# Kernel tuning notes

Measured on AMD Instinct MI355X. Metric: run time of the kernel, lower is better.

## Reference

```python
import jax, jax.numpy as jnp
import numpy as np

B, H, N, D = 16, 2048, 1024, 2048  # batch, seq len, vocab_size, d_model (= 2*vocab)
KAPPA = 1.0
SCALE = 0.02  # std for materialized params (original inits to zeros -> trivial output)


def setup_inputs() -> dict:
    key = jax.random.key(0)
    kz, kf, kv, kw = jax.random.split(key, 4)
    z = jax.random.randint(kz, (B, H), 0, N)
    F_mat = jax.random.normal(kf, (D, D), jnp.float32) * SCALE
    V = jax.random.normal(kv, (D, D), jnp.float32) * SCALE
    W = jax.random.normal(kw, (D, D), jnp.float32) * SCALE
    return {"z": z, "F_mat": F_mat, "V": V, "W": W}


def reference(z, F_mat, V, W):
    # x[b,t] = e_{z[b,t]} + e_{N + z[b,t-1]},  x[b,0] = e_{z[b,0]}  (E / E_tilde basis rows)
    z_prev = jnp.roll(z, 1, axis=1).at[:, 0].set(0)
    E_z = jax.nn.one_hot(z, D, dtype=jnp.float32)          # [B,H,D]
    x = E_z + jax.nn.one_hot(z_prev + N, D, dtype=jnp.float32)
    x = x.at[:, 0, :].set(E_z[:, 0, :])

    x_H = x[:, -1, :]                                      # [B,D] single query
    W_x = jnp.einsum('bhd,ed->bhe', x, W)                  # x @ W.T -> [B,H,D]
    scores = jnp.einsum('bd,bhd->bh', x_H, W_x)            # [B,H]
    attn = jax.nn.softmax(scores, axis=-1)                 # att_type='softmax'
    weighted_sum = jnp.einsum('bh,bhd->bd', attn, x)       # [B,D]

    # U.T @ (.) just takes the first N coordinates (U = E.T, identity columns)
    xi_A = (weighted_sum @ V.T)[:, :N]                     # [B,N]
    combined = x_H + KAPPA * weighted_sum
    xi_F = (combined @ F_mat.T)[:, :N]                     # [B,N]
    xi = xi_A + xi_F
    # match torch output shape [B, N, 1]
    return xi[..., None], xi_A[..., None], xi_F[..., None]
```

## Files before the change

### kernel.cpp

```cpp
#include <hip/hip_runtime.h>

#define BB 16
#define HH 2048
#define NN 1024
#define DD 2048
#define DG4 (DD / 4)


__device__ __forceinline__ unsigned short f2bf(float f) {
    unsigned u = __float_as_uint(f);
    u += 0x7fffu + ((u >> 16) & 1u);
    return (unsigned short)(u >> 16);
}

__global__ __launch_bounds__(512) void ot_p1warm(const int* __restrict__ z,
                                                 const float* __restrict__ Fm,
                                                 const float* __restrict__ Vm,
                                                 const float* __restrict__ Wm,
                                                 int* __restrict__ hdr,
                                                 uint2* __restrict__ wsB) {
    __shared__ int   zsh[HH];
    __shared__ float u[DD];
    __shared__ float wsf[DD];
    __shared__ float redt[8];

    const int tid  = threadIdx.x;
    const int lane = tid & 63;
    const int w    = tid >> 6;
    const int g    = blockIdx.x;

    float4 pf[8];
    {
        const int r = w >> 1, m = w & 1;
        const float4* __restrict__ src =
            (const float4*)((m ? Fm : Vm) + (size_t)(4 * g + r) * DD);
#pragma unroll
        for (int k = 0; k < 8; ++k) pf[k] = src[k * 64 + lane];
    }

    if (g < BB) {
        const int b = g;
        const int4 zt = ((const int4*)(z + (size_t)b * HH))[DG4 - 1];
        const int d1 = zt.w;
        const int d2 = zt.z + NN;

        const int4 zv = ((const int4*)(z + (size_t)b * HH))[tid];
        float4 wa = ((const float4*)(Wm + (size_t)d1 * DD))[tid];
        float4 wc = ((const float4*)(Wm + (size_t)d2 * DD))[tid];

        ((int4*)zsh)[tid] = zv;
        float4 uu;
        uu.x = wa.x + wc.x; uu.y = wa.y + wc.y;
        uu.z = wa.z + wc.z; uu.w = wa.w + wc.w;
        ((float4*)u)[tid] = uu;
        ((float4*)wsf)[tid] = make_float4(0.f, 0.f, 0.f, 0.f);
        __syncthreads();

        const int zp0 = (tid > 0) ? zsh[4 * tid - 1] + NN : 0;
        const float s0 = u[zv.x] + ((tid > 0) ? u[zp0] : 0.f);
        const float s1 = u[zv.y] + u[zv.x + NN];
        const float s2 = u[zv.z] + u[zv.y + NN];
        const float s3 = u[zv.w] + u[zv.z + NN];

        const float e0 = __expf(s0);
        const float e1 = __expf(s1);
        const float e2 = __expf(s2);
        const float e3 = __expf(s3);
        float t = (e0 + e1) + (e2 + e3);
#pragma unroll
        for (int off = 32; off > 0; off >>= 1) t += __shfl_xor(t, off);
        if (lane == 0) redt[w] = t;

        atomicAdd(&wsf[zv.x], e0);
        if (tid > 0) atomicAdd(&wsf[zp0], e0);
        atomicAdd(&wsf[zv.y], e1); atomicAdd(&wsf[zv.x + NN], e1);
        atomicAdd(&wsf[zv.z], e2); atomicAdd(&wsf[zv.y + NN], e2);
        atomicAdd(&wsf[zv.w], e3); atomicAdd(&wsf[zv.z + NN], e3);
        __syncthreads();

        float tot = redt[0];
#pragma unroll
        for (int i = 1; i < 8; ++i) tot += redt[i];
        const float inv = 1.f / tot;

        uint2 p;
        p.x = (unsigned)f2bf(wsf[4 * tid + 0] * inv)
            | ((unsigned)f2bf(wsf[4 * tid + 1] * inv) << 16);
        p.y = (unsigned)f2bf(wsf[4 * tid + 2] * inv)
            | ((unsigned)f2bf(wsf[4 * tid + 3] * inv) << 16);
        wsB[(size_t)tid * BB + b] = p;
        if (tid == 0) { hdr[b] = d1; hdr[BB + b] = d2; }
    }

#pragma unroll
    for (int k = 0; k < 8; ++k)
        asm volatile("" :: "v"(pf[k].x), "v"(pf[k].y), "v"(pf[k].z), "v"(pf[k].w));
}

__global__ __launch_bounds__(512, 4) void ot_phase2(const float* __restrict__ V,
                                                    const float* __restrict__ F,
                                                    const int* __restrict__ hdr,
                                                    const uint2* __restrict__ wsB,
                                                    float* __restrict__ out) {
    const int tid  = threadIdx.x;
    const int lane = tid & 63;
    const int w    = tid >> 6;
    const int b    = lane & 15;
    const int s    = tid >> 4;
    const int g    = blockIdx.x;

    uint2 wsr[16];
#pragma unroll
    for (int i = 0; i < 16; ++i) wsr[i] = wsB[(size_t)(s + 32 * i) * BB + b];

    const float4* __restrict__ Vr0 = (const float4*)(V + (size_t)(4 * g + 0) * DD);
    const float4* __restrict__ Vr1 = (const float4*)(V + (size_t)(4 * g + 1) * DD);
    const float4* __restrict__ Vr2 = (const float4*)(V + (size_t)(4 * g + 2) * DD);
    const float4* __restrict__ Vr3 = (const float4*)(V + (size_t)(4 * g + 3) * DD);
    const float4* __restrict__ Fr0 = (const float4*)(F + (size_t)(4 * g + 0) * DD);
    const float4* __restrict__ Fr1 = (const float4*)(F + (size_t)(4 * g + 1) * DD);
    const float4* __restrict__ Fr2 = (const float4*)(F + (size_t)(4 * g + 2) * DD);
    const float4* __restrict__ Fr3 = (const float4*)(F + (size_t)(4 * g + 3) * DD);

    float acc[8];
#pragma unroll
    for (int j = 0; j < 8; ++j) acc[j] = 0.f;

#pragma unroll
    for (int it = 0; it < 16; ++it) {
        const int dg = s + 32 * it;
        const uint2 p = wsr[it];
        const float s0 = __uint_as_float(p.x << 16);
        const float s1 = __uint_as_float(p.x & 0xffff0000u);
        const float s2 = __uint_as_float(p.y << 16);
        const float s3 = __uint_as_float(p.y & 0xffff0000u);
        float4 v0 = Vr0[dg], v1 = Vr1[dg], v2 = Vr2[dg], v3 = Vr3[dg];
        float4 f0 = Fr0[dg], f1 = Fr1[dg], f2 = Fr2[dg], f3 = Fr3[dg];
        acc[0] += v0.x * s0 + v0.y * s1 + v0.z * s2 + v0.w * s3;
        acc[1] += f0.x * s0 + f0.y * s1 + f0.z * s2 + f0.w * s3;
        acc[2] += v1.x * s0 + v1.y * s1 + v1.z * s2 + v1.w * s3;
        acc[3] += f1.x * s0 + f1.y * s1 + f1.z * s2 + f1.w * s3;
        acc[4] += v2.x * s0 + v2.y * s1 + v2.z * s2 + v2.w * s3;
        acc[5] += f2.x * s0 + f2.y * s1 + f2.z * s2 + f2.w * s3;
        acc[6] += v3.x * s0 + v3.y * s1 + v3.z * s2 + v3.w * s3;
        acc[7] += f3.x * s0 + f3.y * s1 + f3.z * s2 + f3.w * s3;
    }

#pragma unroll
    for (int j = 0; j < 8; ++j) {
        float p = acc[j];
        p += __shfl_xor(p, 16);
        p += __shfl_xor(p, 32);
        acc[j] = p;
    }

    __shared__ float red[8][8][BB];
    if (lane < 16) {
#pragma unroll
        for (int j = 0; j < 8; ++j) red[j][w][b] = acc[j];
    }
    __syncthreads();

    if (tid < 64) {
        const int r = tid >> 4, bb = tid & 15;
        float A = 0.f, Fv = 0.f;
#pragma unroll
        for (int ww = 0; ww < 8; ++ww) {
            A  += red[2 * r + 0][ww][bb];
            Fv += red[2 * r + 1][ww][bb];
        }
        const int n = 4 * g + r;
        const float* __restrict__ Fr = F + (size_t)n * DD;
        Fv += Fr[hdr[bb]] + Fr[hdr[BB + bb]];
        out[(size_t)bb * NN + n]            = A + Fv;
        out[(size_t)(BB + bb) * NN + n]     = A;
        out[(size_t)(2 * BB + bb) * NN + n] = Fv;
    }
}

extern "C" void kernel_launch(void* const* d_in, const int* in_sizes, int n_in,
                              void* d_out, int out_size, void* d_ws, size_t ws_size,
                              hipStream_t stream) {
    const int*   z  = (const int*)d_in[0];
    const float* Fm = (const float*)d_in[1];
    const float* Vm = (const float*)d_in[2];
    const float* Wm = (const float*)d_in[3];
    float* out = (float*)d_out;

    int*   hdr = (int*)d_ws;
    uint2* wsB = (uint2*)((char*)d_ws + 128);

    ot_p1warm<<<256, 512, 0, stream>>>(z, Fm, Vm, Wm, hdr, wsB);
    ot_phase2<<<NN / 4, 512, 0, stream>>>(Vm, Fm, hdr, wsB, out);
}
```

Before: 23.73 us.

## Fuse softmax and projection kernels into one launch with a global flag barrier

Merges the two kernels into a single 256-block launch. The 16 batch blocks publish their bf16 attention weights with atomic stores and bump a release counter, and every block spins on that flag before running the V/F row projection. This removes the second kernel launch and the gap between kernels. In exchange it adds a memset, a spin-wait whose budget can expire, and a dependence on all 256 blocks being co-resident, which is a deadlock or correctness risk.

```diff
diff --git a/kernel.cpp b/kernel.cpp
--- a/kernel.cpp
+++ b/kernel.cpp
@@ -13,16 +13,19 @@
     return (unsigned short)(u >> 16);
 }
 
-__global__ __launch_bounds__(512) void ot_p1warm(const int* __restrict__ z,
-                                                 const float* __restrict__ Fm,
-                                                 const float* __restrict__ Vm,
-                                                 const float* __restrict__ Wm,
-                                                 int* __restrict__ hdr,
-                                                 uint2* __restrict__ wsB) {
+__global__ __launch_bounds__(512) void ot_one(const int* __restrict__ z,
+                                              const float* __restrict__ Fm,
+                                              const float* __restrict__ Vm,
+                                              const float* __restrict__ Wm,
+                                              unsigned* __restrict__ flag,
+                                              int* __restrict__ hdr,
+                                              unsigned long long* __restrict__ wsB,
+                                              float* __restrict__ out) {
     __shared__ int   zsh[HH];
     __shared__ float u[DD];
     __shared__ float wsf[DD];
     __shared__ float redt[8];
+    __shared__ float red[8][8][BB];
 
     const int tid  = threadIdx.x;
     const int lane = tid & 63;
@@ -39,12 +42,12 @@
     }
 
     if (g < BB) {
-        const int b = g;
-        const int4 zt = ((const int4*)(z + (size_t)b * HH))[DG4 - 1];
+        const int b0 = g;
+        const int4 zt = ((const int4*)(z + (size_t)b0 * HH))[DG4 - 1];
         const int d1 = zt.w;
         const int d2 = zt.z + NN;
 
-        const int4 zv = ((const int4*)(z + (size_t)b * HH))[tid];
+        const int4 zv = ((const int4*)(z + (size_t)b0 * HH))[tid];
         float4 wa = ((const float4*)(Wm + (size_t)d1 * DD))[tid];
         float4 wc = ((const float4*)(Wm + (size_t)d2 * DD))[tid];
 
@@ -83,44 +86,53 @@
         for (int i = 1; i < 8; ++i) tot += redt[i];
         const float inv = 1.f / tot;
 
-        uint2 p;
-        p.x = (unsigned)f2bf(wsf[4 * tid + 0] * inv)
-            | ((unsigned)f2bf(wsf[4 * tid + 1] * inv) << 16);
-        p.y = (unsigned)f2bf(wsf[4 * tid + 2] * inv)
-            | ((unsigned)f2bf(wsf[4 * tid + 3] * inv) << 16);
-        wsB[(size_t)tid * BB + b] = p;
-        if (tid == 0) { hdr[b] = d1; hdr[BB + b] = d2; }
-    }
+        const unsigned lo = (unsigned)f2bf(wsf[4 * tid + 0] * inv)
+                          | ((unsigned)f2bf(wsf[4 * tid + 1] * inv) << 16);
+        const unsigned hi = (unsigned)f2bf(wsf[4 * tid + 2] * inv)
+                          | ((unsigned)f2bf(wsf[4 * tid + 3] * inv) << 16);
+        const unsigned long long pk =
+            (unsigned long long)lo | ((unsigned long long)hi << 32);
+        __hip_atomic_store(&wsB[(size_t)tid * BB + b0], pk,
+                           __ATOMIC_RELAXED, __HIP_MEMORY_SCOPE_AGENT);
+        if (tid == 0) {
+            __hip_atomic_store(&hdr[b0], d1, __ATOMIC_RELAXED, __HIP_MEMORY_SCOPE_AGENT);
+            __hip_atomic_store(&hdr[BB + b0], d2, __ATOMIC_RELAXED, __HIP_MEMORY_SCOPE_AGENT);
+        }
+        __syncthreads();
+        if (tid == 0)
+            __hip_atomic_fetch_add(flag, 1u, __ATOMIC_RELEASE, __HIP_MEMORY_SCOPE_AGENT);
+    }
+
+    if (tid == 0) {
+        int budget = 1 << 17;
+        while (__hip_atomic_load(flag, __ATOMIC_RELAXED, __HIP_MEMORY_SCOPE_AGENT) < BB
+               && --budget) {
+            __builtin_amdgcn_s_sleep(8);
+        }
+    }
+    __syncthreads();
 
 #pragma unroll
     for (int k = 0; k < 8; ++k)
         asm volatile("" :: "v"(pf[k].x), "v"(pf[k].y), "v"(pf[k].z), "v"(pf[k].w));
-}
-
-__global__ __launch_bounds__(512, 4) void ot_phase2(const float* __restrict__ V,
-                                                    const float* __restrict__ F,
-                                                    const int* __restrict__ hdr,
-                                                    const uint2* __restrict__ wsB,
-                                                    float* __restrict__ out) {
-    const int tid  = threadIdx.x;
-    const int lane = tid & 63;
-    const int w    = tid >> 6;
-    const int b    = lane & 15;
-    const int s    = tid >> 4;
-    const int g    = blockIdx.x;
-
-    uint2 wsr[16];
-#pragma unroll
-    for (int i = 0; i < 16; ++i) wsr[i] = wsB[(size_t)(s + 32 * i) * BB + b];
-
-    const float4* __restrict__ Vr0 = (const float4*)(V + (size_t)(4 * g + 0) * DD);
-    const float4* __restrict__ Vr1 = (const float4*)(V + (size_t)(4 * g + 1) * DD);
-    const float4* __restrict__ Vr2 = (const float4*)(V + (size_t)(4 * g + 2) * DD);
-    const float4* __restrict__ Vr3 = (const float4*)(V + (size_t)(4 * g + 3) * DD);
-    const float4* __restrict__ Fr0 = (const float4*)(F + (size_t)(4 * g + 0) * DD);
-    const float4* __restrict__ Fr1 = (const float4*)(F + (size_t)(4 * g + 1) * DD);
-    const float4* __restrict__ Fr2 = (const float4*)(F + (size_t)(4 * g + 2) * DD);
-    const float4* __restrict__ Fr3 = (const float4*)(F + (size_t)(4 * g + 3) * DD);
+
+    const int b = lane & 15;
+    const int s = tid >> 4;
+
+    unsigned long long wsr[16];
+#pragma unroll
+    for (int i = 0; i < 16; ++i)
+        wsr[i] = __hip_atomic_load(&wsB[(size_t)(s + 32 * i) * BB + b],
+                                   __ATOMIC_RELAXED, __HIP_MEMORY_SCOPE_AGENT);
+
+    const float4* __restrict__ Vr0 = (const float4*)(Vm + (size_t)(4 * g + 0) * DD);
+    const float4* __restrict__ Vr1 = (const float4*)(Vm + (size_t)(4 * g + 1) * DD);
+    const float4* __restrict__ Vr2 = (const float4*)(Vm + (size_t)(4 * g + 2) * DD);
+    const float4* __restrict__ Vr3 = (const float4*)(Vm + (size_t)(4 * g + 3) * DD);
+    const float4* __restrict__ Fr0 = (const float4*)(Fm + (size_t)(4 * g + 0) * DD);
+    const float4* __restrict__ Fr1 = (const float4*)(Fm + (size_t)(4 * g + 1) * DD);
+    const float4* __restrict__ Fr2 = (const float4*)(Fm + (size_t)(4 * g + 2) * DD);
+    const float4* __restrict__ Fr3 = (const float4*)(Fm + (size_t)(4 * g + 3) * DD);
 
     float acc[8];
 #pragma unroll
@@ -129,11 +141,12 @@
 #pragma unroll
     for (int it = 0; it < 16; ++it) {
         const int dg = s + 32 * it;
-        const uint2 p = wsr[it];
-        const float s0 = __uint_as_float(p.x << 16);
-        const float s1 = __uint_as_float(p.x & 0xffff0000u);
-        const float s2 = __uint_as_float(p.y << 16);
-        const float s3 = __uint_as_float(p.y & 0xffff0000u);
+        const unsigned px = (unsigned)wsr[it];
+        const unsigned py = (unsigned)(wsr[it] >> 32);
+        const float s0 = __uint_as_float(px << 16);
+        const float s1 = __uint_as_float(px & 0xffff0000u);
+        const float s2 = __uint_as_float(py << 16);
+        const float s3 = __uint_as_float(py & 0xffff0000u);
         float4 v0 = Vr0[dg], v1 = Vr1[dg], v2 = Vr2[dg], v3 = Vr3[dg];
         float4 f0 = Fr0[dg], f1 = Fr1[dg], f2 = Fr2[dg], f3 = Fr3[dg];
         acc[0] += v0.x * s0 + v0.y * s1 + v0.z * s2 + v0.w * s3;
@@ -154,7 +167,6 @@
         acc[j] = p;
     }
 
-    __shared__ float red[8][8][BB];
     if (lane < 16) {
 #pragma unroll
         for (int j = 0; j < 8; ++j) red[j][w][b] = acc[j];
@@ -170,8 +182,10 @@
             Fv += red[2 * r + 1][ww][bb];
         }
         const int n = 4 * g + r;
-        const float* __restrict__ Fr = F + (size_t)n * DD;
-        Fv += Fr[hdr[bb]] + Fr[hdr[BB + bb]];
+        const int e1i = __hip_atomic_load(&hdr[bb],      __ATOMIC_RELAXED, __HIP_MEMORY_SCOPE_AGENT);
+        const int e2i = __hip_atomic_load(&hdr[BB + bb], __ATOMIC_RELAXED, __HIP_MEMORY_SCOPE_AGENT);
+        const float* __restrict__ Fr = Fm + (size_t)n * DD;
+        Fv += Fr[e1i] + Fr[e2i];
         out[(size_t)bb * NN + n]            = A + Fv;
         out[(size_t)(BB + bb) * NN + n]     = A;
         out[(size_t)(2 * BB + bb) * NN + n] = Fv;
@@ -187,9 +201,10 @@
     const float* Wm = (const float*)d_in[3];
     float* out = (float*)d_out;
 
-    int*   hdr = (int*)d_ws;
-    uint2* wsB = (uint2*)((char*)d_ws + 128);
-
-    ot_p1warm<<<256, 512, 0, stream>>>(z, Fm, Vm, Wm, hdr, wsB);
-    ot_phase2<<<NN / 4, 512, 0, stream>>>(Vm, Fm, hdr, wsB, out);
+    unsigned* flag = (unsigned*)d_ws;
+    int*      hdr  = (int*)((char*)d_ws + 128);
+    unsigned long long* wsB = (unsigned long long*)((char*)d_ws + 256);
+
+    hipMemsetAsync(flag, 0, sizeof(unsigned), stream);
+    ot_one<<<256, 512, 0, stream>>>(z, Fm, Vm, Wm, flag, hdr, wsB, out);
 }
```

Measured after the change: 30.61 us. 1.29x slower.
